# Optimization experiments

Measured on AMD Instinct MI355X. Metric: run time of the kernel, lower is better.

## Reference

```python
import jax, jax.numpy as jnp
import numpy as np

B, N, T, L, H = 8, 128, 256, 32, 128


def setup_inputs() -> dict:
    key = jax.random.key(0)
    k0, k1, k2, k3, k4, k5 = jax.random.split(key, 6)
    x = jax.random.uniform(k0, (B, N, T), dtype=jnp.float32)
    s = 1.0 / np.sqrt(H)  # pytorch LSTM/Linear default init scale
    W_ih = jax.random.uniform(k1, (N, 4 * H, L), minval=-s, maxval=s, dtype=jnp.float32)
    b_ih = jax.random.uniform(k2, (N, 4 * H), minval=-s, maxval=s, dtype=jnp.float32)
    b_hh = jax.random.uniform(k3, (N, 4 * H), minval=-s, maxval=s, dtype=jnp.float32)
    W_fc = jax.random.uniform(k4, (N, N, H), minval=-s, maxval=s, dtype=jnp.float32)  # [node_i, out_j, H]
    b_fc = jax.random.uniform(k5, (N, N), minval=-s, maxval=s, dtype=jnp.float32)  # [node_i, out_j]
    return {"x": x, "W_ih": W_ih, "b_ih": b_ih, "b_hh": b_hh, "W_fc": W_fc, "b_fc": b_fc}


def reference(x, W_ih, b_ih, b_hh, W_fc, b_fc):
    # x: [B, N, T]
    Bn, Nn, Tn = x.shape
    Ln = W_ih.shape[-1]
    Hh = W_fc.shape[-1]
    Ttau = Tn - Ln  # number of prediction steps (t = L .. T-1)

    # Sliding windows x[:, i, tau:tau+L] for tau = 0..Ttau-1  -> [B, N, Ttau, L]
    idx = jnp.arange(Ttau)[:, None] + jnp.arange(Ln)[None, :]  # [Ttau, L]
    xw = x[:, :, idx]

    # Single-step LSTM with zero initial state: W_hh term vanishes.
    gates = jnp.einsum('bntl,ngl->bntg', xw, W_ih) + (b_ih + b_hh)[None, :, None, :]
    gi, gf, gg, go = jnp.split(gates, 4, axis=-1)  # pytorch order: i, f, g, o
    c = jax.nn.sigmoid(gi) * jnp.tanh(gg)          # f*c0 = 0
    h = jax.nn.sigmoid(go) * jnp.tanh(c)           # [B, N, Ttau, H]

    # Per-node fc (grouped GEMM): contributions[b, tau, j, i]
    contrib = jnp.einsum('bnth,njh->btjn', h, W_fc) + b_fc.T[None, None, :, :]

    # G[b, j, i] = mean_tau contrib[b, tau, j, i] / x[b, i, L + tau]
    denom = jnp.transpose(x[:, :, Ln:], (0, 2, 1))[:, :, None, :]  # [B, Ttau, 1, N_i]
    G = jnp.mean(contrib / denom, axis=1)                          # [B, N, N]

    X_hat = jnp.sum(contrib, axis=2) + 1e-6  # [B, Ttau, N]
    return G, X_hat
```

## Files before the change

### kernel.cpp

```cpp
#include <hip/hip_runtime.h>
#include <math.h>

#define B_  8
#define N_  128
#define T_  256
#define L_  32
#define H_  128
#define TT_ 224

typedef float f4  __attribute__((ext_vector_type(4)));
typedef float f32x4 __attribute__((ext_vector_type(4)));
typedef short bf16x8 __attribute__((ext_vector_type(8)));

__device__ __forceinline__ float fsig(float x) {
    return __builtin_amdgcn_rcpf(1.0f + __expf(-x));
}
__device__ __forceinline__ float ftanh_(float x) {
    return 1.0f - 2.0f * __builtin_amdgcn_rcpf(1.0f + __expf(2.0f * x));
}
__device__ __forceinline__ unsigned pk2bf(float a, float b) {
    unsigned ua = __float_as_uint(a), ub = __float_as_uint(b);
    ua = (ua + 0x7FFFu + ((ua >> 16) & 1u)) >> 16;
    ub = (ub + 0x7FFFu + ((ub >> 16) & 1u)) >> 16;
    return ua | (ub << 16);
}

__global__ __launch_bounds__(512)
void k_pre(const float* __restrict__ W_fc, const float* __restrict__ b_fc,
           const float* __restrict__ W_ih, const float* __restrict__ b_ih,
           const float* __restrict__ b_hh,
           float* __restrict__ wsum, float* __restrict__ bsum,
           unsigned short* __restrict__ W3g, float* __restrict__ bia_g) {
    const int n  = blockIdx.x;
    const int h  = threadIdx.x & 127;
    const int jq = threadIdx.x >> 7;
    const float* W = W_fc + (size_t)n * N_ * H_ + (size_t)jq * 32 * H_;
    float s = 0.f;
    #pragma unroll 8
    for (int j = 0; j < 32; ++j) s += W[j * H_ + h];
    __shared__ float part[4][128];
    __shared__ float bp[2];
    part[jq][h] = s;

    if (threadIdx.x < 128) {
        float bv = b_fc[n * N_ + threadIdx.x];
        #pragma unroll
        for (int off = 32; off > 0; off >>= 1) bv += __shfl_down(bv, off, 64);
        if ((threadIdx.x & 63) == 0) bp[threadIdx.x >> 6] = bv;
    }
    __syncthreads();
    if (threadIdx.x < 128)
        wsum[n * H_ + h] = part[0][h] + part[1][h] + part[2][h] + part[3][h];
    if (threadIdx.x == 0) bsum[n] = bp[0] + bp[1];

    const f4* Wi = (const f4*)(W_ih + (size_t)n * 4 * H_ * L_);
    for (int i = threadIdx.x; i < 3072; i += 512) {
        const int r  = i >> 3;
        const int c4 = i & 7;
        const int sr = r + (r >= 128 ? 128 : 0);
        f4 v = Wi[sr * 8 + c4];
        unsigned2_t: ;
        unsigned p0 = pk2bf(v.x, v.y), p1 = pk2bf(v.z, v.w);
        *(uint2*)&W3g[(size_t)n * 12288 + r * 32 + c4 * 4] = make_uint2(p0, p1);
    }
    for (int i = threadIdx.x; i < 384; i += 512) {
        const int sr = i + (i >= 128 ? 128 : 0);
        bia_g[n * 384 + i] = b_ih[(size_t)n * 4 * H_ + sr] + b_hh[(size_t)n * 4 * H_ + sr];
    }
}

__global__ __launch_bounds__(256)
__attribute__((amdgpu_waves_per_eu(4, 4)))
void k_main(const float* __restrict__ x,
            const unsigned short* __restrict__ W3g,
            const float* __restrict__ bia_g,
            const float* __restrict__ wsum, const float* __restrict__ bsum,
            float* __restrict__ Hd, float* __restrict__ Dinv,
            float* __restrict__ xhat) {
    const int n   = blockIdx.x;
    const int b   = blockIdx.y;
    const int tid = threadIdx.x;
    const int w    = tid >> 6;
    const int lane = tid & 63;
    const int col  = lane & 15;
    const int quad = lane >> 4;

    __shared__ unsigned short W3[384 * 40];
    __shared__ float xs[258];
    __shared__ unsigned xeo[2][128];
    __shared__ float xr[TT_];
    __shared__ float bia_s[384];
    __shared__ float ws_s[H_];
    __shared__ float xh_part[4][TT_];
    __shared__ float red[4];

    {
        const ushort4* src4 = (const ushort4*)(W3g + (size_t)n * 12288);
        #pragma unroll
        for (int k = 0; k < 12; ++k) {
            const int i = tid + k * 256;
            const int r = i >> 3, c = (i & 7) * 4;
            *(ushort4*)&W3[r * 40 + c] = src4[i];
        }
    }
    if (tid < 256) xs[tid] = x[((size_t)b * N_ + n) * T_ + tid];
    if (tid < 2)   xs[256 + tid] = 0.f;
    if (tid < 128) ws_s[tid] = wsum[n * H_ + tid];
    for (int i = tid; i < 384; i += 256) bia_s[i] = bia_g[n * 384 + i];
    __syncthreads();
    if (tid < TT_) xr[tid] = 1.0f / xs[L_ + tid];
    if (tid < 128) {
        xeo[0][tid] = pk2bf(xs[2 * tid],     xs[2 * tid + 1]);
        xeo[1][tid] = pk2bf(xs[2 * tid + 1], xs[2 * tid + 2]);
    }
    __syncthreads();

    bf16x8 bfr[2][3];
    float  biaL[2][3], wshL[2];
    #pragma unroll
    for (int ht2 = 0; ht2 < 2; ++ht2) {
        const int ht = 2 * w + ht2;
        #pragma unroll
        for (int g = 0; g < 3; ++g) {
            const int row = g * 128 + ht * 16 + col;
            bfr[ht2][g]  = *(const bf16x8*)&W3[row * 40 + quad * 8];
            biaL[ht2][g] = bia_s[g * 128 + ht * 16 + col];
        }
        wshL[ht2] = ws_s[ht * 16 + col];
    }

    float hd_acc[2] = {0.f, 0.f};
    const f32x4 zero4 = {0.f, 0.f, 0.f, 0.f};

    for (int ttile = 0; ttile < 14; ++ttile) {
        const int s = ttile * 16 + col + quad * 8;
        const int p = s & 1, base = s >> 1;
        union { unsigned u[4]; bf16x8 v; } af;
        #pragma unroll
        for (int q = 0; q < 4; ++q) af.u[q] = xeo[p][base + q];

        const f4 xr4 = *(const f4*)&xr[ttile * 16 + quad * 4];
        float px[4] = {0.f, 0.f, 0.f, 0.f};

        #pragma unroll
        for (int ht2 = 0; ht2 < 2; ++ht2) {
            f32x4 ai = __builtin_amdgcn_mfma_f32_16x16x32_bf16(af.v, bfr[ht2][0], zero4, 0, 0, 0);
            f32x4 ag = __builtin_amdgcn_mfma_f32_16x16x32_bf16(af.v, bfr[ht2][1], zero4, 0, 0, 0);
            f32x4 ao = __builtin_amdgcn_mfma_f32_16x16x32_bf16(af.v, bfr[ht2][2], zero4, 0, 0, 0);
            #pragma unroll
            for (int reg = 0; reg < 4; ++reg) {
                const float gi = ai[reg] + biaL[ht2][0];
                const float gg = ag[reg] + biaL[ht2][1];
                const float go = ao[reg] + biaL[ht2][2];
                const float c  = fsig(gi) * ftanh_(gg);
                const float hh = fsig(go) * ftanh_(c);
                hd_acc[ht2] = fmaf(hh, xr4[reg], hd_acc[ht2]);
                px[reg]     = fmaf(hh, wshL[ht2], px[reg]);
            }
        }
        #pragma unroll
        for (int reg = 0; reg < 4; ++reg) {
            float pv = px[reg];
            pv += __shfl_xor(pv, 1, 64);
            pv += __shfl_xor(pv, 2, 64);
            pv += __shfl_xor(pv, 4, 64);
            pv += __shfl_xor(pv, 8, 64);
            if (col == 0) xh_part[w][ttile * 16 + quad * 4 + reg] = pv;
        }
    }

    #pragma unroll
    for (int ht2 = 0; ht2 < 2; ++ht2) {
        float v = hd_acc[ht2];
        v += __shfl_xor(v, 16, 64);
        v += __shfl_xor(v, 32, 64);
        if (lane < 16)
            Hd[((size_t)b * N_ + n) * H_ + (2 * w + ht2) * 16 + lane] = v;
    }

    __syncthreads();
    if (tid < TT_) {
        const float v = xh_part[0][tid] + xh_part[1][tid] +
                        xh_part[2][tid] + xh_part[3][tid];
        xhat[((size_t)b * TT_ + tid) * N_ + n] = v + bsum[n] + 1e-6f;
    }
    float dv = (tid < TT_) ? xr[tid] : 0.f;
    #pragma unroll
    for (int off = 32; off > 0; off >>= 1) dv += __shfl_down(dv, off, 64);
    if (lane == 0) red[w] = dv;
    __syncthreads();
    if (tid == 0) Dinv[b * N_ + n] = red[0] + red[1] + red[2] + red[3];
}

__global__ __launch_bounds__(256)
void k_g(const float* __restrict__ W_fc, const float* __restrict__ b_fc,
         const float* __restrict__ Hd, const float* __restrict__ Dinv,
         float* __restrict__ G) {
    const int n = blockIdx.x;
    __shared__ f4 wrow[128 * 33];
    __shared__ float hd_s[B_][H_];
    __shared__ float dinv_s[B_];
    __shared__ float pacc[128][B_];

    const f4* Wg = (const f4*)(W_fc + (size_t)n * N_ * H_);
    for (int i = threadIdx.x; i < 4096; i += 256) {
        const int j = i >> 5, c = i & 31;
        wrow[j * 33 + c] = Wg[i];
    }
    for (int i = threadIdx.x; i < B_ * H_; i += 256)
        hd_s[i >> 7][i & 127] = Hd[((size_t)(i >> 7) * N_ + n) * H_ + (i & 127)];
    if (threadIdx.x < B_) dinv_s[threadIdx.x] = Dinv[threadIdx.x * N_ + n];
    __syncthreads();

    const int j   = threadIdx.x & 127;
    const int hh2 = threadIdx.x >> 7;
    float acc[B_];
    #pragma unroll
    for (int bb = 0; bb < B_; ++bb) acc[bb] = 0.f;
    #pragma unroll
    for (int q = 0; q < 16; ++q) {
        const f4 w = wrow[j * 33 + hh2 * 16 + q];
        const int hb = hh2 * 64 + q * 4;
        #pragma unroll
        for (int bb = 0; bb < B_; ++bb) {
            acc[bb] = fmaf(w[0], hd_s[bb][hb + 0],
                      fmaf(w[1], hd_s[bb][hb + 1],
                      fmaf(w[2], hd_s[bb][hb + 2],
                      fmaf(w[3], hd_s[bb][hb + 3], acc[bb]))));
        }
    }
    if (hh2 == 1) {
        #pragma unroll
        for (int bb = 0; bb < B_; ++bb) pacc[j][bb] = acc[bb];
    }
    __syncthreads();
    if (hh2 == 0) {
        const float bj  = b_fc[n * N_ + j];
        const float inv = 1.0f / 224.0f;
        #pragma unroll
        for (int bb = 0; bb < B_; ++bb)
            G[(size_t)bb * N_ * N_ + (size_t)j * N_ + n] =
                (acc[bb] + pacc[j][bb] + bj * dinv_s[bb]) * inv;
    }
}

extern "C" void kernel_launch(void* const* d_in, const int* in_sizes, int n_in,
                              void* d_out, int out_size, void* d_ws, size_t ws_size,
                              hipStream_t stream) {
    const float* x    = (const float*)d_in[0];
    const float* W_ih = (const float*)d_in[1];
    const float* b_ih = (const float*)d_in[2];
    const float* b_hh = (const float*)d_in[3];
    const float* W_fc = (const float*)d_in[4];
    const float* b_fc = (const float*)d_in[5];

    float* G    = (float*)d_out;
    float* xhat = (float*)d_out + (size_t)B_ * N_ * N_;

    float* wsum = (float*)d_ws;
    float* bsum = wsum + N_ * H_;
    float* Hd   = bsum + N_;
    float* Dinv = Hd + (size_t)B_ * N_ * H_;
    float* bia_g = Dinv + B_ * N_;
    unsigned short* W3g = (unsigned short*)(bia_g + N_ * 384);

    k_pre<<<dim3(N_), dim3(512), 0, stream>>>(W_fc, b_fc, W_ih, b_ih, b_hh,
                                              wsum, bsum, W3g, bia_g);
    k_main<<<dim3(N_, B_), dim3(256), 0, stream>>>(x, W3g, bia_g,
                                                   wsum, bsum, Hd, Dinv, xhat);
    k_g<<<dim3(N_), dim3(256), 0, stream>>>(W_fc, b_fc, Hd, Dinv, G);
}
```

Before: 128.4 us.

## Fuse weight preprocessing into main kernel and split G kernel across output rows

Removes the separate preprocessing kernel: each main-kernel block now loads W_ih directly, converts it to bf16 in shared memory, sums W_fc rows and b_fc itself, and computes the gate biases. This saves one launch and the global round trip of the converted weights, at the cost of redundant per-batch recomputation (8x) of the W_fc column sums and the conversion. The G kernel is re-gridded to 16-row tiles of W_fc per block (8x more blocks) with a shared-memory reduction, which raises parallelism for that small GEMM.

```diff
diff --git a/kernel.cpp b/kernel.cpp
--- a/kernel.cpp
+++ b/kernel.cpp
@@ -8,7 +8,7 @@
 #define H_  128
 #define TT_ 224
 
-typedef float f4  __attribute__((ext_vector_type(4)));
+typedef float f4    __attribute__((ext_vector_type(4)));
 typedef float f32x4 __attribute__((ext_vector_type(4)));
 typedef short bf16x8 __attribute__((ext_vector_type(8)));
 
@@ -25,56 +25,11 @@
     return ua | (ub << 16);
 }
 
-__global__ __launch_bounds__(512)
-void k_pre(const float* __restrict__ W_fc, const float* __restrict__ b_fc,
-           const float* __restrict__ W_ih, const float* __restrict__ b_ih,
-           const float* __restrict__ b_hh,
-           float* __restrict__ wsum, float* __restrict__ bsum,
-           unsigned short* __restrict__ W3g, float* __restrict__ bia_g) {
-    const int n  = blockIdx.x;
-    const int h  = threadIdx.x & 127;
-    const int jq = threadIdx.x >> 7;
-    const float* W = W_fc + (size_t)n * N_ * H_ + (size_t)jq * 32 * H_;
-    float s = 0.f;
-    #pragma unroll 8
-    for (int j = 0; j < 32; ++j) s += W[j * H_ + h];
-    __shared__ float part[4][128];
-    __shared__ float bp[2];
-    part[jq][h] = s;
-
-    if (threadIdx.x < 128) {
-        float bv = b_fc[n * N_ + threadIdx.x];
-        #pragma unroll
-        for (int off = 32; off > 0; off >>= 1) bv += __shfl_down(bv, off, 64);
-        if ((threadIdx.x & 63) == 0) bp[threadIdx.x >> 6] = bv;
-    }
-    __syncthreads();
-    if (threadIdx.x < 128)
-        wsum[n * H_ + h] = part[0][h] + part[1][h] + part[2][h] + part[3][h];
-    if (threadIdx.x == 0) bsum[n] = bp[0] + bp[1];
-
-    const f4* Wi = (const f4*)(W_ih + (size_t)n * 4 * H_ * L_);
-    for (int i = threadIdx.x; i < 3072; i += 512) {
-        const int r  = i >> 3;
-        const int c4 = i & 7;
-        const int sr = r + (r >= 128 ? 128 : 0);
-        f4 v = Wi[sr * 8 + c4];
-        unsigned2_t: ;
-        unsigned p0 = pk2bf(v.x, v.y), p1 = pk2bf(v.z, v.w);
-        *(uint2*)&W3g[(size_t)n * 12288 + r * 32 + c4 * 4] = make_uint2(p0, p1);
-    }
-    for (int i = threadIdx.x; i < 384; i += 512) {
-        const int sr = i + (i >= 128 ? 128 : 0);
-        bia_g[n * 384 + i] = b_ih[(size_t)n * 4 * H_ + sr] + b_hh[(size_t)n * 4 * H_ + sr];
-    }
-}
-
 __global__ __launch_bounds__(256)
 __attribute__((amdgpu_waves_per_eu(4, 4)))
-void k_main(const float* __restrict__ x,
-            const unsigned short* __restrict__ W3g,
-            const float* __restrict__ bia_g,
-            const float* __restrict__ wsum, const float* __restrict__ bsum,
+void k_main(const float* __restrict__ x, const float* __restrict__ W_ih,
+            const float* __restrict__ b_ih, const float* __restrict__ b_hh,
+            const float* __restrict__ W_fc, const float* __restrict__ b_fc,
             float* __restrict__ Hd, float* __restrict__ Dinv,
             float* __restrict__ xhat) {
     const int n   = blockIdx.x;
@@ -93,25 +48,52 @@
     __shared__ float ws_s[H_];
     __shared__ float xh_part[4][TT_];
     __shared__ float red[4];
+    __shared__ float bsum_s;
+
+    float* bfv   = &xh_part[0][0];
+    float* part2 = &xh_part[1][0];
 
     {
-        const ushort4* src4 = (const ushort4*)(W3g + (size_t)n * 12288);
+        const f4* Wi = (const f4*)(W_ih + (size_t)n * 4 * H_ * L_);
         #pragma unroll
         for (int k = 0; k < 12; ++k) {
-            const int i = tid + k * 256;
-            const int r = i >> 3, c = (i & 7) * 4;
-            *(ushort4*)&W3[r * 40 + c] = src4[i];
-        }
-    }
+            const int i  = tid + k * 256;
+            const int r  = i >> 3;
+            const int c4 = i & 7;
+            const int sr = r + (r >= 128 ? 128 : 0);
+            f4 v = Wi[sr * 8 + c4];
+            unsigned p0 = pk2bf(v.x, v.y), p1 = pk2bf(v.z, v.w);
+            *(uint2*)&W3[r * 40 + c4 * 4] = make_uint2(p0, p1);
+        }
+    }
+    {
+        const int h = tid & 127, jq = tid >> 7;
+        const float* Wf = W_fc + (size_t)n * N_ * H_ + (size_t)jq * 64 * H_ + h;
+        float s = 0.f;
+        #pragma unroll 8
+        for (int j = 0; j < 64; ++j) s += Wf[j * H_];
+        part2[jq * 128 + h] = s;
+    }
+    for (int i = tid; i < 384; i += 256) {
+        const int sr = i + (i >= 128 ? 128 : 0);
+        bia_s[i] = b_ih[(size_t)n * 4 * H_ + sr] + b_hh[(size_t)n * 4 * H_ + sr];
+    }
+    if (tid < 128) bfv[tid] = b_fc[n * N_ + tid];
     if (tid < 256) xs[tid] = x[((size_t)b * N_ + n) * T_ + tid];
     if (tid < 2)   xs[256 + tid] = 0.f;
-    if (tid < 128) ws_s[tid] = wsum[n * H_ + tid];
-    for (int i = tid; i < 384; i += 256) bia_s[i] = bia_g[n * 384 + i];
-    __syncthreads();
+    __syncthreads();
+
     if (tid < TT_) xr[tid] = 1.0f / xs[L_ + tid];
     if (tid < 128) {
         xeo[0][tid] = pk2bf(xs[2 * tid],     xs[2 * tid + 1]);
         xeo[1][tid] = pk2bf(xs[2 * tid + 1], xs[2 * tid + 2]);
+    }
+    if (tid < 128) ws_s[tid] = part2[tid] + part2[128 + tid];
+    if (tid < 64) {
+        float t = bfv[tid] + bfv[tid + 64];
+        #pragma unroll
+        for (int off = 32; off > 0; off >>= 1) t += __shfl_down(t, off, 64);
+        if (tid == 0) bsum_s = t;
     }
     __syncthreads();
 
@@ -182,7 +164,7 @@
     if (tid < TT_) {
         const float v = xh_part[0][tid] + xh_part[1][tid] +
                         xh_part[2][tid] + xh_part[3][tid];
-        xhat[((size_t)b * TT_ + tid) * N_ + n] = v + bsum[n] + 1e-6f;
+        xhat[((size_t)b * TT_ + tid) * N_ + n] = v + bsum_s + 1e-6f;
     }
     float dv = (tid < TT_) ? xr[tid] : 0.f;
     #pragma unroll
@@ -196,51 +178,55 @@
 void k_g(const float* __restrict__ W_fc, const float* __restrict__ b_fc,
          const float* __restrict__ Hd, const float* __restrict__ Dinv,
          float* __restrict__ G) {
-    const int n = blockIdx.x;
-    __shared__ f4 wrow[128 * 33];
-    __shared__ float hd_s[B_][H_];
+    const int n  = blockIdx.x;
+    const int j0 = blockIdx.y * 16;
+    const int tid = threadIdx.x;
+
+    __shared__ float ws[16][132];
+    __shared__ float hd_s[B_][132];
     __shared__ float dinv_s[B_];
-    __shared__ float pacc[128][B_];
-
-    const f4* Wg = (const f4*)(W_fc + (size_t)n * N_ * H_);
-    for (int i = threadIdx.x; i < 4096; i += 256) {
-        const int j = i >> 5, c = i & 31;
-        wrow[j * 33 + c] = Wg[i];
-    }
-    for (int i = threadIdx.x; i < B_ * H_; i += 256)
+    __shared__ float pacc[16][16][8];
+
+    const f4* Wg = (const f4*)(W_fc + ((size_t)n * N_ + j0) * H_);
+    #pragma unroll
+    for (int k = 0; k < 2; ++k) {
+        const int i = tid + k * 256;
+        *(f4*)&ws[i >> 5][(i & 31) * 4] = Wg[i];
+    }
+    for (int i = tid; i < B_ * H_; i += 256)
         hd_s[i >> 7][i & 127] = Hd[((size_t)(i >> 7) * N_ + n) * H_ + (i & 127)];
-    if (threadIdx.x < B_) dinv_s[threadIdx.x] = Dinv[threadIdx.x * N_ + n];
-    __syncthreads();
-
-    const int j   = threadIdx.x & 127;
-    const int hh2 = threadIdx.x >> 7;
+    if (tid < B_) dinv_s[tid] = Dinv[tid * N_ + n];
+    __syncthreads();
+
+    const int jl  = tid >> 4;
+    const int cl  = tid & 15;
     float acc[B_];
     #pragma unroll
     for (int bb = 0; bb < B_; ++bb) acc[bb] = 0.f;
     #pragma unroll
-    for (int q = 0; q < 16; ++q) {
-        const f4 w = wrow[j * 33 + hh2 * 16 + q];
-        const int hb = hh2 * 64 + q * 4;
+    for (int q = 0; q < 2; ++q) {
+        const f4 wv = *(const f4*)&ws[jl][cl * 8 + q * 4];
+        const int hb = cl * 8 + q * 4;
         #pragma unroll
         for (int bb = 0; bb < B_; ++bb) {
-            acc[bb] = fmaf(w[0], hd_s[bb][hb + 0],
-                      fmaf(w[1], hd_s[bb][hb + 1],
-                      fmaf(w[2], hd_s[bb][hb + 2],
-                      fmaf(w[3], hd_s[bb][hb + 3], acc[bb]))));
-        }
-    }
-    if (hh2 == 1) {
-        #pragma unroll
-        for (int bb = 0; bb < B_; ++bb) pacc[j][bb] = acc[bb];
-    }
-    __syncthreads();
-    if (hh2 == 0) {
-        const float bj  = b_fc[n * N_ + j];
-        const float inv = 1.0f / 224.0f;
-        #pragma unroll
-        for (int bb = 0; bb < B_; ++bb)
-            G[(size_t)bb * N_ * N_ + (size_t)j * N_ + n] =
-                (acc[bb] + pacc[j][bb] + bj * dinv_s[bb]) * inv;
+            acc[bb] = fmaf(wv.x, hd_s[bb][hb + 0],
+                      fmaf(wv.y, hd_s[bb][hb + 1],
+                      fmaf(wv.z, hd_s[bb][hb + 2],
+                      fmaf(wv.w, hd_s[bb][hb + 3], acc[bb]))));
+        }
+    }
+    #pragma unroll
+    for (int bb = 0; bb < B_; ++bb) pacc[jl][cl][bb] = acc[bb];
+    __syncthreads();
+
+    if (tid < 128) {
+        const int j2 = tid >> 3, bb = tid & 7;
+        float s = 0.f;
+        #pragma unroll
+        for (int c = 0; c < 16; ++c) s += pacc[j2][c][bb];
+        const float bj = b_fc[n * N_ + j0 + j2];
+        G[(size_t)bb * N_ * N_ + (size_t)(j0 + j2) * N_ + n] =
+            (s + bj * dinv_s[bb]) * (1.0f / 224.0f);
     }
 }
 
@@ -257,16 +243,10 @@
     float* G    = (float*)d_out;
     float* xhat = (float*)d_out + (size_t)B_ * N_ * N_;
 
-    float* wsum = (float*)d_ws;
-    float* bsum = wsum + N_ * H_;
-    float* Hd   = bsum + N_;
+    float* Hd   = (float*)d_ws;
     float* Dinv = Hd + (size_t)B_ * N_ * H_;
-    float* bia_g = Dinv + B_ * N_;
-    unsigned short* W3g = (unsigned short*)(bia_g + N_ * 384);
-
-    k_pre<<<dim3(N_), dim3(512), 0, stream>>>(W_fc, b_fc, W_ih, b_ih, b_hh,
-                                              wsum, bsum, W3g, bia_g);
-    k_main<<<dim3(N_, B_), dim3(256), 0, stream>>>(x, W3g, bia_g,
-                                                   wsum, bsum, Hd, Dinv, xhat);
-    k_g<<<dim3(N_), dim3(256), 0, stream>>>(W_fc, b_fc, Hd, Dinv, G);
-}
+
+    k_main<<<dim3(N_, B_), dim3(256), 0, stream>>>(x, W_ih, b_ih, b_hh,
+                                                   W_fc, b_fc, Hd, Dinv, xhat);
+    k_g<<<dim3(N_, 8), dim3(256), 0, stream>>>(W_fc, b_fc, Hd, Dinv, G);
+}
```

Measured after the change: 120.0 us. 6.6% less time.
